# Kernel optimization log

Measured on AMD Instinct MI355X. Metric: run time of the kernel, lower is better.

The kernel has to match this reference:

```python
import jax, jax.numpy as jnp
import numpy as np

K = 16          # neighbors (min(k, N) with N=1024 -> 16)
HID = 64        # hidden_dim
NFEAT = 64      # num_features
LN_EPS = 1e-5


def _block(h, W, b, g, beta, a):
    # Linear -> LayerNorm -> PReLU (single shared slope a, torch default)
    h = jnp.einsum('...i,oi->...o', h, W) + b
    mu = jnp.mean(h, axis=-1, keepdims=True)
    var = jnp.mean((h - mu) ** 2, axis=-1, keepdims=True)
    h = g * (h - mu) / jnp.sqrt(var + LN_EPS) + beta
    return jnp.where(h > 0, h, a * h)


def setup_inputs() -> dict:
    key = jax.random.key(0)
    ks = jax.random.split(key, 12)
    B, N, D, F, H = 16, 1024, 3, NFEAT, HID
    points = jax.random.normal(ks[0], (B, N, D), dtype=jnp.float32)
    x = jax.random.normal(ks[1], (B, N, F), dtype=jnp.float32)
    mask = jax.random.randint(ks[2], (B, N), 0, 2, dtype=jnp.int32)
    s0 = 1.0 / np.sqrt(2 * F)
    sh = 1.0 / np.sqrt(H)
    W0 = jax.random.uniform(ks[3], (H, 2 * F), jnp.float32, -s0, s0)
    b0 = jax.random.uniform(ks[4], (H,), jnp.float32, -s0, s0)
    Wh = jax.random.uniform(ks[5], (4, H, H), jnp.float32, -sh, sh)  # 3 hidden + 1 final
    bh = jax.random.uniform(ks[6], (4, H), jnp.float32, -sh, sh)
    ln_g = jnp.ones((5, H), dtype=jnp.float32)
    ln_b = jnp.zeros((5, H), dtype=jnp.float32)
    prelu_a = jnp.full((5,), 0.25, dtype=jnp.float32)
    return {"points": points, "x": x, "mask": mask, "W0": W0, "b0": b0,
            "Wh": Wh, "bh": bh, "ln_g": ln_g, "ln_b": ln_b, "prelu_a": prelu_a}


def reference(points, x, mask, W0, b0, Wh, bh, ln_g, ln_b, prelu_a):
    B, N, _ = points.shape
    F = x.shape[-1]
    # pairwise euclidean distances, invalid columns -> +inf
    delta = points[:, :, None, :] - points[:, None, :, :]          # [B,N,N,D]
    dist = jnp.sqrt(jnp.sum(delta * delta, axis=-1))               # [B,N,N]
    dist = jnp.where(mask.astype(bool)[:, None, :], dist, jnp.inf)
    # k smallest distances -> neighbor indices
    _, idx = jax.lax.top_k(-dist, K)                               # [B,N,K]
    n_tracks = jnp.sum(mask.astype(jnp.float32), axis=-1)          # [B]
    neighbors = x[jnp.arange(B)[:, None, None], idx]               # [B,N,K,F]
    xc = jnp.broadcast_to(x[:, :, None, :], (B, N, K, F))
    h = jnp.concatenate([xc, x[:, :, None, :] - neighbors], axis=-1)  # [B,N,K,2F]
    h = _block(h, W0, b0, ln_g[0], ln_b[0], prelu_a[0])
    for i in range(4):
        h = _block(h, Wh[i], bh[i], ln_g[i + 1], ln_b[i + 1], prelu_a[i + 1])
    # masked mean over neighbor slots (mask uses original n_tracks)
    nm = (jnp.arange(K)[None, None, :] < n_tracks[:, None, None]).astype(jnp.float32)  # [B,N,K]
    n_safe = jnp.where(n_tracks == 0, 1.0, n_tracks)
    aggregated = jnp.sum(h * nm[..., None], axis=-2) / n_safe[:, None, None]
    return aggregated
```

## Files before the change

### kernel.cpp

```cpp
#include <hip/hip_runtime.h>
#include <hip/hip_bf16.h>
#include <math.h>

#define N_ 1024
#define KNN_K 16
#define LN_EPS 1e-5f

typedef unsigned long long u64;
typedef unsigned int u32;
typedef __attribute__((ext_vector_type(4))) float f32x4;
typedef __attribute__((ext_vector_type(8))) short short8;
typedef __attribute__((ext_vector_type(2))) unsigned int u32x2;
typedef __attribute__((ext_vector_type(4))) unsigned int u32x4;

__device__ __forceinline__ u32 rn_hi32(float v) {
  u32 u = __float_as_uint(v);
  return (u + 0x7FFFu + ((u >> 16) & 1u)) & 0xFFFF0000u;
}
__device__ __forceinline__ u32 rn_b16(float v) {
  u32 u = __float_as_uint(v);
  return (u + 0x7FFFu + ((u >> 16) & 1u)) >> 16;
}

__global__ __launch_bounds__(256) void front_kernel(
    const float* __restrict__ Wh, u32x4* __restrict__ whi,
    u32x4* __restrict__ wlo, const int* __restrict__ mask,
    float* __restrict__ ntr, const float* __restrict__ points,
    int* __restrict__ knn, const float* __restrict__ x,
    const float* __restrict__ W0, const float* __restrict__ b0,
    float* __restrict__ p_c, float* __restrict__ p_n) {
  __shared__ float SM[8192];
  const int blk = blockIdx.x;
  const int t = threadIdx.x;

  if (blk < 8) {
    int idx = blk * 256 + t;
    int lane = idx & 63;
    int ks = (idx >> 6) & 1;
    int m = (idx >> 7) & 3;
    int li = idx >> 9;
    int o = 16 * m + (lane & 15);
    int k0 = 32 * ks + 8 * (lane >> 4);
    const float* w = Wh + li * 4096 + o * 64 + k0;
    u32x4 hi, lo;
#pragma unroll
    for (int j = 0; j < 4; j++) {
      float f0 = w[2 * j], f1 = w[2 * j + 1];
      u32 h0 = rn_hi32(f0);
      u32 h1 = rn_hi32(f1);
      float l0 = f0 - __uint_as_float(h0);
      float l1 = f1 - __uint_as_float(h1);
      hi[j] = (h0 >> 16) | h1;
      lo[j] = rn_b16(l0) | (rn_b16(l1) << 16);
    }
    int fi = ((li * 4 + m) * 2 + ks) * 64 + lane;
    whi[fi] = hi;
    wlo[fi] = lo;
  } else if (blk < 24) {
    int b = blk - 8;
    int s = 0;
    for (int e = t; e < N_; e += 256) s += mask[b * N_ + e];
    for (int off = 32; off; off >>= 1) s += __shfl_xor(s, off, 64);
    int* accI = (int*)SM;
    int wave = t >> 6, lane = t & 63;
    if (lane == 0) accI[wave] = s;
    __syncthreads();
    if (t == 0) ntr[b] = (float)(accI[0] + accI[1] + accI[2] + accI[3]);
  } else if (blk < 24 + 4096) {
#pragma clang fp contract(off)
    float* px = SM;
    float* py = SM + 1024;
    float* pz = SM + 2048;
    float* minf = SM + 3072;
    int kb = blk - 24;
    int b = kb >> 8;
    int qbase = (kb & 255) << 2;
    for (int j = t; j < N_; j += 256) {
      const float* p = points + ((size_t)(b * N_ + j)) * 3;
      px[j] = p[0];
      py[j] = p[1];
      pz[j] = p[2];
      minf[j] = mask[b * N_ + j] ? 0.0f : __builtin_inff();
    }
    __syncthreads();
    int wave = t >> 6, lane = t & 63;
    int n = qbase + wave;
    float qx = px[n], qy = py[n], qz = pz[n];
    u64 key[16];
#pragma unroll
    for (int c = 0; c < 16; c++) {
      int j = lane + (c << 6);
      float dx = qx - px[j];
      float dy = qy - py[j];
      float dz = qz - pz[j];
      float d2 = dx * dx + dy * dy + dz * dz;
      d2 = d2 + minf[j];
      key[c] = ((u64)__float_as_uint(d2) << 32) | (u32)j;
    }
    int* dst = knn + ((size_t)(b * N_ + n)) * KNN_K;
    for (int s = 0; s < 16; s++) {
      u64 m = key[0];
#pragma unroll
      for (int c = 1; c < 16; c++) m = key[c] < m ? key[c] : m;
#pragma unroll
      for (int off = 32; off; off >>= 1) {
        u64 o = __shfl_xor(m, off, 64);
        if (o < m) m = o;
      }
      if (lane == 0) dst[s] = (int)(m & 0xFFFFFFFFu);
#pragma unroll
      for (int c = 0; c < 16; c++)
        if (key[c] == m) key[c] = ~0ULL;
    }
  } else {
    float* Wc = SM;
    float* Wn = SM + 4096;
    int pb = blk - (24 + 4096);
    for (int e = t; e < 4096; e += 256) {
      int o = e & 63, i = e >> 6;
      float wa = W0[o * 128 + i];
      float wb = W0[o * 128 + 64 + i];
      Wc[i * 64 + o] = wa + wb;
      Wn[i * 64 + o] = wb;
    }
    __syncthreads();
    int wave = t >> 6, lane = t & 63;
    int pbase = pb * 64 + wave * 16;
    for (int it = 0; it < 16; it++) {
      int p = pbase + it;
      const float* xr = x + (size_t)__builtin_amdgcn_readfirstlane(p) * 64;
      float pc = b0[lane];
      float pn = 0.0f;
#pragma unroll
      for (int i = 0; i < 64; i++) {
        float xi = xr[i];
        pc = fmaf(xi, Wc[i * 64 + lane], pc);
        pn = fmaf(xi, Wn[i * 64 + lane], pn);
      }
      p_c[(size_t)p * 64 + lane] = pc;
      p_n[(size_t)p * 64 + lane] = pn;
    }
  }
}

__global__ __launch_bounds__(256) void layer0_kernel(
    const float* __restrict__ p_c, const float* __restrict__ p_n,
    const int* __restrict__ knn_, const float* __restrict__ ln_g,
    const float* __restrict__ ln_b, const float* __restrict__ prelu_a,
    u32* __restrict__ Hout) {
  int e = blockIdx.x * 256 + threadIdx.x;
  int p = e >> 4;
  int b = p >> 10;
  int j = knn_[e];
  const f32x4* pc4 = (const f32x4*)(p_c + (size_t)p * 64);
  const f32x4* pn4 = (const f32x4*)(p_n + (size_t)((b << 10) + j) * 64);
  float h[64];
#pragma unroll
  for (int q = 0; q < 16; q++) {
    f32x4 a = pc4[q], v = pn4[q];
    h[q * 4 + 0] = a[0] - v[0];
    h[q * 4 + 1] = a[1] - v[1];
    h[q * 4 + 2] = a[2] - v[2];
    h[q * 4 + 3] = a[3] - v[3];
  }
  float s = 0.0f, s2 = 0.0f;
#pragma unroll
  for (int o = 0; o < 64; o++) { s += h[o]; s2 += h[o] * h[o]; }
  float mu = s * (1.0f / 64.0f);
  float var = s2 * (1.0f / 64.0f) - mu * mu;
  float inv = rsqrtf(var + LN_EPS);
  float aslope = prelu_a[0];
#pragma unroll
  for (int o = 0; o < 64; o++) {
    float v = ln_g[o] * ((h[o] - mu) * inv) + ln_b[o];
    h[o] = v > 0.0f ? v : aslope * v;
  }
  u32 pk[32];
#pragma unroll
  for (int w = 0; w < 32; w++)
    pk[w] = rn_b16(h[2 * w]) | (rn_b16(h[2 * w + 1]) << 16);
  u32x4* dst = (u32x4*)(Hout + (size_t)e * 32);
#pragma unroll
  for (int q = 0; q < 8; q++) {
    u32x4 v;
    v[0] = pk[4 * q + 0];
    v[1] = pk[4 * q + 1];
    v[2] = pk[4 * q + 2];
    v[3] = pk[4 * q + 3];
    dst[q] = v;
  }
}

__global__ __launch_bounds__(128) void layer_kernel(
    const u32* __restrict__ Hin, u32* __restrict__ Hout,
    const u32x4* __restrict__ whi, const u32x4* __restrict__ wlo,
    const float* __restrict__ bh, const float* __restrict__ ln_g,
    const float* __restrict__ ln_b, const float* __restrict__ prelu_a,
    const float* __restrict__ ntr, float* __restrict__ out, int li, int last) {
  const int t = threadIdx.x;
  const int wv = t >> 6, l = t & 63;
  const int c = l & 15;
  const int g = l >> 4;
  const int pbase = blockIdx.x * 8 + wv * 4;
  const int b = pbase >> 10;

  u32x4 bw[4][2];
#pragma unroll
  for (int nt = 0; nt < 4; nt++) {
    size_t eb = ((size_t)(pbase + nt) * 16 + c) * 32;
#pragma unroll
    for (int ks = 0; ks < 2; ks++)
      bw[nt][ks] = *(const u32x4*)(Hin + eb + 16 * ks + 4 * g);
  }

  f32x4 bias4[4];
#pragma unroll
  for (int m = 0; m < 4; m++)
    bias4[m] = *(const f32x4*)(bh + li * 64 + 16 * m + 4 * g);

  f32x4 acc[4][4];
#pragma unroll
  for (int m = 0; m < 4; m++)
#pragma unroll
    for (int nt = 0; nt < 4; nt++) acc[m][nt] = bias4[m];

#pragma unroll
  for (int ks = 0; ks < 2; ks++)
#pragma unroll
    for (int m = 0; m < 4; m++) {
      int fi = ((li * 4 + m) * 2 + ks) * 64 + l;
      short8 ah = __builtin_bit_cast(short8, whi[fi]);
      short8 al = __builtin_bit_cast(short8, wlo[fi]);
#pragma unroll
      for (int nt = 0; nt < 4; nt++) {
        short8 bb = __builtin_bit_cast(short8, bw[nt][ks]);
        acc[m][nt] = __builtin_amdgcn_mfma_f32_16x16x32_bf16(ah, bb, acc[m][nt], 0, 0, 0);
        acc[m][nt] = __builtin_amdgcn_mfma_f32_16x16x32_bf16(al, bb, acc[m][nt], 0, 0, 0);
      }
    }

  f32x4 g4[4], b4[4];
#pragma unroll
  for (int m = 0; m < 4; m++) {
    g4[m] = *(const f32x4*)(ln_g + (li + 1) * 64 + 16 * m + 4 * g);
    b4[m] = *(const f32x4*)(ln_b + (li + 1) * 64 + 16 * m + 4 * g);
  }
  float aslope = prelu_a[li + 1];
#pragma unroll
  for (int nt = 0; nt < 4; nt++) {
    float s = 0.0f, s2 = 0.0f;
#pragma unroll
    for (int m = 0; m < 4; m++)
#pragma unroll
      for (int v = 0; v < 4; v++) {
        float x = acc[m][nt][v];
        s += x;
        s2 = fmaf(x, x, s2);
      }
    s += __shfl_xor(s, 16, 64);
    s2 += __shfl_xor(s2, 16, 64);
    s += __shfl_xor(s, 32, 64);
    s2 += __shfl_xor(s2, 32, 64);
    float mu = s * (1.0f / 64.0f);
    float var = s2 * (1.0f / 64.0f) - mu * mu;
    float inv = rsqrtf(var + LN_EPS);
#pragma unroll
    for (int m = 0; m < 4; m++)
#pragma unroll
      for (int v = 0; v < 4; v++) {
        float x = (acc[m][nt][v] - mu) * inv;
        x = g4[m][v] * x + b4[m][v];
        acc[m][nt][v] = x > 0.0f ? x : aslope * x;
      }
  }

  if (!last) {
#pragma unroll
    for (int nt = 0; nt < 4; nt++) {
      size_t eb = ((size_t)(pbase + nt) * 16 + c) * 32;
#pragma unroll
      for (int m = 0; m < 4; m++) {
        u32x2 v;
        v[0] = rn_b16(acc[m][nt][0]) | (rn_b16(acc[m][nt][1]) << 16);
        v[1] = rn_b16(acc[m][nt][2]) | (rn_b16(acc[m][nt][3]) << 16);
        *(u32x2*)(Hout + eb + 8 * m + 2 * g) = v;
      }
    }
  } else {
    float cnt = ntr[b];
    float n_safe = (cnt == 0.0f) ? 1.0f : cnt;
    float rinv = 1.0f / n_safe;
    float msk = ((float)c < cnt) ? 1.0f : 0.0f;
#pragma unroll
    for (int nt = 0; nt < 4; nt++)
#pragma unroll
      for (int m = 0; m < 4; m++) {
        f32x4 r;
#pragma unroll
        for (int v = 0; v < 4; v++) {
          float x = acc[m][nt][v] * msk;
          x += __shfl_xor(x, 1, 64);
          x += __shfl_xor(x, 2, 64);
          x += __shfl_xor(x, 4, 64);
          x += __shfl_xor(x, 8, 64);
          r[v] = x * rinv;
        }
        if (c == 0)
          *(f32x4*)(out + (size_t)(pbase + nt) * 64 + 16 * m + 4 * g) = r;
      }
  }
}

__global__ __launch_bounds__(128) void mlp_mfma3_kernel(
    const float* __restrict__ p_c, const float* __restrict__ p_n,
    const int* __restrict__ knn_, const u32x4* __restrict__ whi,
    const u32x4* __restrict__ wlo, const float* __restrict__ bh,
    const float* __restrict__ ln_g, const float* __restrict__ ln_b,
    const float* __restrict__ prelu_a, const float* __restrict__ ntr,
    float* __restrict__ out) {
  const int t = threadIdx.x;
  const int wv = t >> 6, l = t & 63;
  const int c = l & 15;
  const int g = l >> 4;
  const int pbase = blockIdx.x * 8 + wv * 4;
  const int b = pbase >> 10;

  u32x4 bhi[4][2], blo[4][2];

  {
    float h[64];
    int p0 = pbase + g;
    int j = knn_[(size_t)p0 * 16 + c];
    const float4* pc4 = reinterpret_cast<const float4*>(p_c + (size_t)p0 * 64);
    const float4* pn4 = reinterpret_cast<const float4*>(p_n + (size_t)((b << 10) + j) * 64);
#pragma unroll
    for (int q = 0; q < 16; q++) {
      float4 a = pc4[q], v = pn4[q];
      h[q * 4 + 0] = a.x - v.x;
      h[q * 4 + 1] = a.y - v.y;
      h[q * 4 + 2] = a.z - v.z;
      h[q * 4 + 3] = a.w - v.w;
    }
    float s = 0.0f, s2 = 0.0f;
#pragma unroll
    for (int o = 0; o < 64; o++) { s += h[o]; s2 += h[o] * h[o]; }
    float mu = s * (1.0f / 64.0f);
    float var = s2 * (1.0f / 64.0f) - mu * mu;
    float inv = rsqrtf(var + LN_EPS);
    float aslope = prelu_a[0];
#pragma unroll
    for (int o = 0; o < 64; o++) {
      float v = ln_g[o] * ((h[o] - mu) * inv) + ln_b[o];
      h[o] = v > 0.0f ? v : aslope * v;
    }
    u32 hpk_hi[32], hpk_lo[32];
#pragma unroll
    for (int w = 0; w < 32; w++) {
      float f0 = h[2 * w], f1 = h[2 * w + 1];
      u32 h0 = rn_hi32(f0);
      u32 h1 = rn_hi32(f1);
      float l0 = f0 - __uint_as_float(h0);
      float l1 = f1 - __uint_as_float(h1);
      hpk_hi[w] = (h0 >> 16) | h1;
      hpk_lo[w] = rn_b16(l0) | (rn_b16(l1) << 16);
    }
#pragma unroll
    for (int nt = 0; nt < 4; nt++) {
      int src = c + 16 * nt;
#pragma unroll
      for (int ks = 0; ks < 2; ks++)
#pragma unroll
        for (int gw = 0; gw < 4; gw++)
#pragma unroll
          for (int j2 = 0; j2 < 4; j2++) {
            u32 th = (u32)__shfl((int)hpk_hi[16 * ks + 4 * gw + j2], src, 64);
            u32 tl = (u32)__shfl((int)hpk_lo[16 * ks + 4 * gw + j2], src, 64);
            if (g == gw) {
              bhi[nt][ks][j2] = th;
              blo[nt][ks][j2] = tl;
            }
          }
    }
  }

  float cnt = ntr[b];

#pragma unroll 1
  for (int li = 0; li < 4; li++) {
    f32x4 bias4[4];
#pragma unroll
    for (int m = 0; m < 4; m++)
      bias4[m] = *(const f32x4*)(bh + li * 64 + 16 * m + 4 * g);

    f32x4 acc[4][4];
#pragma unroll
    for (int m = 0; m < 4; m++)
#pragma unroll
      for (int nt = 0; nt < 4; nt++) acc[m][nt] = bias4[m];

#pragma unroll
    for (int ks = 0; ks < 2; ks++)
#pragma unroll
      for (int m = 0; m < 4; m++) {
        int fi = ((li * 4 + m) * 2 + ks) * 64 + l;
        short8 ah = __builtin_bit_cast(short8, whi[fi]);
        short8 al = __builtin_bit_cast(short8, wlo[fi]);
#pragma unroll
        for (int nt = 0; nt < 4; nt++) {
          short8 bh_ = __builtin_bit_cast(short8, bhi[nt][ks]);
          short8 bl_ = __builtin_bit_cast(short8, blo[nt][ks]);
          acc[m][nt] = __builtin_amdgcn_mfma_f32_16x16x32_bf16(ah, bh_, acc[m][nt], 0, 0, 0);
          acc[m][nt] = __builtin_amdgcn_mfma_f32_16x16x32_bf16(ah, bl_, acc[m][nt], 0, 0, 0);
          acc[m][nt] = __builtin_amdgcn_mfma_f32_16x16x32_bf16(al, bh_, acc[m][nt], 0, 0, 0);
        }
      }

    f32x4 g4[4], b4[4];
#pragma unroll
    for (int m = 0; m < 4; m++) {
      g4[m] = *(const f32x4*)(ln_g + (li + 1) * 64 + 16 * m + 4 * g);
      b4[m] = *(const f32x4*)(ln_b + (li + 1) * 64 + 16 * m + 4 * g);
    }
    float aslope = prelu_a[li + 1];
#pragma unroll
    for (int nt = 0; nt < 4; nt++) {
      float s = 0.0f, s2 = 0.0f;
#pragma unroll
      for (int m = 0; m < 4; m++)
#pragma unroll
        for (int v = 0; v < 4; v++) {
          float x = acc[m][nt][v];
          s += x;
          s2 = fmaf(x, x, s2);
        }
      s += __shfl_xor(s, 16, 64);
      s2 += __shfl_xor(s2, 16, 64);
      s += __shfl_xor(s, 32, 64);
      s2 += __shfl_xor(s2, 32, 64);
      float mu = s * (1.0f / 64.0f);
      float var = s2 * (1.0f / 64.0f) - mu * mu;
      float inv = rsqrtf(var + LN_EPS);
#pragma unroll
      for (int m = 0; m < 4; m++)
#pragma unroll
        for (int v = 0; v < 4; v++) {
          float x = (acc[m][nt][v] - mu) * inv;
          x = g4[m][v] * x + b4[m][v];
          acc[m][nt][v] = x > 0.0f ? x : aslope * x;
        }
    }

    if (li < 3) {
      float h[64];
#pragma unroll
      for (int o = 0; o < 64; o++) {
        int srcl = c + 16 * ((o >> 2) & 3);
#pragma unroll
        for (int ntp = 0; ntp < 4; ntp++) {
          float tv = __shfl(acc[o >> 4][ntp][o & 3], srcl, 64);
          if (g == ntp) h[o] = tv;
        }
      }
      u32 hpk_hi[32], hpk_lo[32];
#pragma unroll
      for (int w = 0; w < 32; w++) {
        float f0 = h[2 * w], f1 = h[2 * w + 1];
        u32 h0 = rn_hi32(f0);
        u32 h1 = rn_hi32(f1);
        float l0 = f0 - __uint_as_float(h0);
        float l1 = f1 - __uint_as_float(h1);
        hpk_hi[w] = (h0 >> 16) | h1;
        hpk_lo[w] = rn_b16(l0) | (rn_b16(l1) << 16);
      }
#pragma unroll
      for (int nt = 0; nt < 4; nt++) {
        int src = c + 16 * nt;
#pragma unroll
        for (int ks = 0; ks < 2; ks++)
#pragma unroll
          for (int gw = 0; gw < 4; gw++)
#pragma unroll
            for (int j2 = 0; j2 < 4; j2++) {
              u32 th = (u32)__shfl((int)hpk_hi[16 * ks + 4 * gw + j2], src, 64);
              u32 tl = (u32)__shfl((int)hpk_lo[16 * ks + 4 * gw + j2], src, 64);
              if (g == gw) {
                bhi[nt][ks][j2] = th;
                blo[nt][ks][j2] = tl;
              }
            }
      }
    } else {
      float n_safe = (cnt == 0.0f) ? 1.0f : cnt;
      float rinv = 1.0f / n_safe;
      float msk = ((float)c < cnt) ? 1.0f : 0.0f;
#pragma unroll
      for (int nt = 0; nt < 4; nt++)
#pragma unroll
        for (int m = 0; m < 4; m++) {
          f32x4 r;
#pragma unroll
          for (int v = 0; v < 4; v++) {
            float x = acc[m][nt][v] * msk;
            x += __shfl_xor(x, 1, 64);
            x += __shfl_xor(x, 2, 64);
            x += __shfl_xor(x, 4, 64);
            x += __shfl_xor(x, 8, 64);
            r[v] = x * rinv;
          }
          if (c == 0)
            *(f32x4*)(out + (size_t)(pbase + nt) * 64 + 16 * m + 4 * g) = r;
        }
    }
  }
}

extern "C" void kernel_launch(void* const* d_in, const int* in_sizes, int n_in,
                              void* d_out, int out_size, void* d_ws, size_t ws_size,
                              hipStream_t stream) {
  const float* points  = (const float*)d_in[0];
  const float* x       = (const float*)d_in[1];
  const int*   mask    = (const int*)d_in[2];
  const float* W0      = (const float*)d_in[3];
  const float* b0      = (const float*)d_in[4];
  const float* Wh      = (const float*)d_in[5];
  const float* bh      = (const float*)d_in[6];
  const float* ln_g    = (const float*)d_in[7];
  const float* ln_b    = (const float*)d_in[8];
  const float* prelu_a = (const float*)d_in[9];
  float* out = (float*)d_out;

  char* ws = (char*)d_ws;
  int*   knn  = (int*)ws;
  float* p_c  = (float*)(ws + (1 << 20));
  float* p_n  = (float*)(ws + (1 << 20) + (4 << 20));
  u32x4* whi  = (u32x4*)(ws + (9 << 20));
  u32x4* wlo  = (u32x4*)(ws + (9 << 20) + (32 << 10));
  float* ntr  = (float*)(ws + (9 << 20) + (64 << 10));
  u32*   H0   = (u32*)(ws + ((size_t)10 << 20));
  u32*   H1   = (u32*)(ws + ((size_t)42 << 20));

  front_kernel<<<24 + 4096 + 256, 256, 0, stream>>>(
      Wh, whi, wlo, mask, ntr, points, knn, x, W0, b0, p_c, p_n);

  if (ws_size >= ((size_t)74 << 20)) {
    layer0_kernel<<<1024, 256, 0, stream>>>(p_c, p_n, knn, ln_g, ln_b, prelu_a, H0);
    layer_kernel<<<2048, 128, 0, stream>>>(H0, H1, whi, wlo, bh, ln_g, ln_b,
                                           prelu_a, ntr, out, 0, 0);
    layer_kernel<<<2048, 128, 0, stream>>>(H1, H0, whi, wlo, bh, ln_g, ln_b,
                                           prelu_a, ntr, out, 1, 0);
    layer_kernel<<<2048, 128, 0, stream>>>(H0, H1, whi, wlo, bh, ln_g, ln_b,
                                           prelu_a, ntr, out, 2, 0);
    layer_kernel<<<2048, 128, 0, stream>>>(H1, H0, whi, wlo, bh, ln_g, ln_b,
                                           prelu_a, ntr, out, 3, 1);
  } else {
    mlp_mfma3_kernel<<<2048, 128, 0, stream>>>(p_c, p_n, knn, whi, wlo, bh,
                                               ln_g, ln_b, prelu_a, ntr, out);
  }
}
```

Before: 200.5 us.

## Fuse layer-0 LayerNorm/PReLU with first hidden MFMA layer into one kernel

Merges the layer-0 kernel (gather, LN, PReLU, bf16 store) with the first hidden Linear+LN+PReLU layer. The layer-0 activations stay in registers as hi/lo bf16 splits and are redistributed to the MFMA B-operand layout through wave shuffles. This removes one kernel launch and one full write and read of the edge activation buffer. In exchange it adds many shuffles and uses more registers per thread.

```diff
diff --git a/kernel.cpp b/kernel.cpp
--- a/kernel.cpp
+++ b/kernel.cpp
@@ -143,51 +143,151 @@
   }
 }
 
-__global__ __launch_bounds__(256) void layer0_kernel(
+__global__ __launch_bounds__(128) void layerA_kernel(
     const float* __restrict__ p_c, const float* __restrict__ p_n,
-    const int* __restrict__ knn_, const float* __restrict__ ln_g,
-    const float* __restrict__ ln_b, const float* __restrict__ prelu_a,
-    u32* __restrict__ Hout) {
-  int e = blockIdx.x * 256 + threadIdx.x;
-  int p = e >> 4;
-  int b = p >> 10;
-  int j = knn_[e];
-  const f32x4* pc4 = (const f32x4*)(p_c + (size_t)p * 64);
-  const f32x4* pn4 = (const f32x4*)(p_n + (size_t)((b << 10) + j) * 64);
-  float h[64];
-#pragma unroll
-  for (int q = 0; q < 16; q++) {
-    f32x4 a = pc4[q], v = pn4[q];
-    h[q * 4 + 0] = a[0] - v[0];
-    h[q * 4 + 1] = a[1] - v[1];
-    h[q * 4 + 2] = a[2] - v[2];
-    h[q * 4 + 3] = a[3] - v[3];
-  }
-  float s = 0.0f, s2 = 0.0f;
-#pragma unroll
-  for (int o = 0; o < 64; o++) { s += h[o]; s2 += h[o] * h[o]; }
-  float mu = s * (1.0f / 64.0f);
-  float var = s2 * (1.0f / 64.0f) - mu * mu;
-  float inv = rsqrtf(var + LN_EPS);
-  float aslope = prelu_a[0];
-#pragma unroll
-  for (int o = 0; o < 64; o++) {
-    float v = ln_g[o] * ((h[o] - mu) * inv) + ln_b[o];
-    h[o] = v > 0.0f ? v : aslope * v;
-  }
-  u32 pk[32];
-#pragma unroll
-  for (int w = 0; w < 32; w++)
-    pk[w] = rn_b16(h[2 * w]) | (rn_b16(h[2 * w + 1]) << 16);
-  u32x4* dst = (u32x4*)(Hout + (size_t)e * 32);
-#pragma unroll
-  for (int q = 0; q < 8; q++) {
-    u32x4 v;
-    v[0] = pk[4 * q + 0];
-    v[1] = pk[4 * q + 1];
-    v[2] = pk[4 * q + 2];
-    v[3] = pk[4 * q + 3];
-    dst[q] = v;
+    const int* __restrict__ knn_, const u32x4* __restrict__ whi,
+    const u32x4* __restrict__ wlo, const float* __restrict__ bh,
+    const float* __restrict__ ln_g, const float* __restrict__ ln_b,
+    const float* __restrict__ prelu_a, u32* __restrict__ Hout) {
+  const int t = threadIdx.x;
+  const int wv = t >> 6, l = t & 63;
+  const int c = l & 15;
+  const int g = l >> 4;
+  const int pbase = blockIdx.x * 8 + wv * 4;
+  const int b = pbase >> 10;
+
+  u32x4 bhi[4][2], blo[4][2];
+
+  {
+    float h[64];
+    int p0 = pbase + g;
+    int j = knn_[(size_t)p0 * 16 + c];
+    const float4* pc4 = reinterpret_cast<const float4*>(p_c + (size_t)p0 * 64);
+    const float4* pn4 = reinterpret_cast<const float4*>(p_n + (size_t)((b << 10) + j) * 64);
+#pragma unroll
+    for (int q = 0; q < 16; q++) {
+      float4 a = pc4[q], v = pn4[q];
+      h[q * 4 + 0] = a.x - v.x;
+      h[q * 4 + 1] = a.y - v.y;
+      h[q * 4 + 2] = a.z - v.z;
+      h[q * 4 + 3] = a.w - v.w;
+    }
+    float s = 0.0f, s2 = 0.0f;
+#pragma unroll
+    for (int o = 0; o < 64; o++) { s += h[o]; s2 += h[o] * h[o]; }
+    float mu = s * (1.0f / 64.0f);
+    float var = s2 * (1.0f / 64.0f) - mu * mu;
+    float inv = rsqrtf(var + LN_EPS);
+    float aslope = prelu_a[0];
+#pragma unroll
+    for (int o = 0; o < 64; o++) {
+      float v = ln_g[o] * ((h[o] - mu) * inv) + ln_b[o];
+      h[o] = v > 0.0f ? v : aslope * v;
+    }
+    u32 hpk_hi[32], hpk_lo[32];
+#pragma unroll
+    for (int w = 0; w < 32; w++) {
+      float f0 = h[2 * w], f1 = h[2 * w + 1];
+      u32 h0 = rn_hi32(f0);
+      u32 h1 = rn_hi32(f1);
+      float l0 = f0 - __uint_as_float(h0);
+      float l1 = f1 - __uint_as_float(h1);
+      hpk_hi[w] = (h0 >> 16) | h1;
+      hpk_lo[w] = rn_b16(l0) | (rn_b16(l1) << 16);
+    }
+#pragma unroll
+    for (int nt = 0; nt < 4; nt++) {
+      int src = c + 16 * nt;
+#pragma unroll
+      for (int ks = 0; ks < 2; ks++)
+#pragma unroll
+        for (int gw = 0; gw < 4; gw++)
+#pragma unroll
+          for (int j2 = 0; j2 < 4; j2++) {
+            u32 th = (u32)__shfl((int)hpk_hi[16 * ks + 4 * gw + j2], src, 64);
+            u32 tl = (u32)__shfl((int)hpk_lo[16 * ks + 4 * gw + j2], src, 64);
+            if (g == gw) {
+              bhi[nt][ks][j2] = th;
+              blo[nt][ks][j2] = tl;
+            }
+          }
+    }
+  }
+
+  const int li = 0;
+  f32x4 bias4[4];
+#pragma unroll
+  for (int m = 0; m < 4; m++)
+    bias4[m] = *(const f32x4*)(bh + li * 64 + 16 * m + 4 * g);
+
+  f32x4 acc[4][4];
+#pragma unroll
+  for (int m = 0; m < 4; m++)
+#pragma unroll
+    for (int nt = 0; nt < 4; nt++) acc[m][nt] = bias4[m];
+
+#pragma unroll
+  for (int ks = 0; ks < 2; ks++)
+#pragma unroll
+    for (int m = 0; m < 4; m++) {
+      int fi = ((li * 4 + m) * 2 + ks) * 64 + l;
+      short8 ah = __builtin_bit_cast(short8, whi[fi]);
+      short8 al = __builtin_bit_cast(short8, wlo[fi]);
+#pragma unroll
+      for (int nt = 0; nt < 4; nt++) {
+        short8 bh_ = __builtin_bit_cast(short8, bhi[nt][ks]);
+        short8 bl_ = __builtin_bit_cast(short8, blo[nt][ks]);
+        acc[m][nt] = __builtin_amdgcn_mfma_f32_16x16x32_bf16(ah, bh_, acc[m][nt], 0, 0, 0);
+        acc[m][nt] = __builtin_amdgcn_mfma_f32_16x16x32_bf16(ah, bl_, acc[m][nt], 0, 0, 0);
+        acc[m][nt] = __builtin_amdgcn_mfma_f32_16x16x32_bf16(al, bh_, acc[m][nt], 0, 0, 0);
+      }
+    }
+
+  f32x4 g4[4], b4[4];
+#pragma unroll
+  for (int m = 0; m < 4; m++) {
+    g4[m] = *(const f32x4*)(ln_g + (li + 1) * 64 + 16 * m + 4 * g);
+    b4[m] = *(const f32x4*)(ln_b + (li + 1) * 64 + 16 * m + 4 * g);
+  }
+  float aslope = prelu_a[li + 1];
+#pragma unroll
+  for (int nt = 0; nt < 4; nt++) {
+    float s = 0.0f, s2 = 0.0f;
+#pragma unroll
+    for (int m = 0; m < 4; m++)
+#pragma unroll
+      for (int v = 0; v < 4; v++) {
+        float x = acc[m][nt][v];
+        s += x;
+        s2 = fmaf(x, x, s2);
+      }
+    s += __shfl_xor(s, 16, 64);
+    s2 += __shfl_xor(s2, 16, 64);
+    s += __shfl_xor(s, 32, 64);
+    s2 += __shfl_xor(s2, 32, 64);
+    float mu = s * (1.0f / 64.0f);
+    float var = s2 * (1.0f / 64.0f) - mu * mu;
+    float inv = rsqrtf(var + LN_EPS);
+#pragma unroll
+    for (int m = 0; m < 4; m++)
+#pragma unroll
+      for (int v = 0; v < 4; v++) {
+        float x = (acc[m][nt][v] - mu) * inv;
+        x = g4[m][v] * x + b4[m][v];
+        acc[m][nt][v] = x > 0.0f ? x : aslope * x;
+      }
+  }
+
+#pragma unroll
+  for (int nt = 0; nt < 4; nt++) {
+    size_t eb = ((size_t)(pbase + nt) * 16 + c) * 32;
+#pragma unroll
+    for (int m = 0; m < 4; m++) {
+      u32x2 v;
+      v[0] = rn_b16(acc[m][nt][0]) | (rn_b16(acc[m][nt][1]) << 16);
+      v[1] = rn_b16(acc[m][nt][2]) | (rn_b16(acc[m][nt][3]) << 16);
+      *(u32x2*)(Hout + eb + 8 * m + 2 * g) = v;
+    }
   }
 }
 
@@ -543,14 +643,13 @@
       Wh, whi, wlo, mask, ntr, points, knn, x, W0, b0, p_c, p_n);
 
   if (ws_size >= ((size_t)74 << 20)) {
-    layer0_kernel<<<1024, 256, 0, stream>>>(p_c, p_n, knn, ln_g, ln_b, prelu_a, H0);
+    layerA_kernel<<<2048, 128, 0, stream>>>(p_c, p_n, knn, whi, wlo, bh,
+                                            ln_g, ln_b, prelu_a, H0);
     layer_kernel<<<2048, 128, 0, stream>>>(H0, H1, whi, wlo, bh, ln_g, ln_b,
-                                           prelu_a, ntr, out, 0, 0);
+                                           prelu_a, ntr, out, 1, 0);
     layer_kernel<<<2048, 128, 0, stream>>>(H1, H0, whi, wlo, bh, ln_g, ln_b,
-                                           prelu_a, ntr, out, 1, 0);
+                                           prelu_a, ntr, out, 2, 0);
     layer_kernel<<<2048, 128, 0, stream>>>(H0, H1, whi, wlo, bh, ln_g, ln_b,
-                                           prelu_a, ntr, out, 2, 0);
-    layer_kernel<<<2048, 128, 0, stream>>>(H1, H0, whi, wlo, bh, ln_g, ln_b,
                                            prelu_a, ntr, out, 3, 1);
   } else {
     mlp_mfma3_kernel<<<2048, 128, 0, stream>>>(p_c, p_n, knn, whi, wlo, bh,
```

New measurement: 199.0 us. Within noise of the previous version (-0.8%).
